# Kernel optimization log

Measured on AMD Instinct MI355X. Metric: run time of the kernel, lower is better.

Reference implementation:

```python
import jax, jax.numpy as jnp
import numpy as np

PS = 8          # patch_size
NF = 64         # num_feat
HEADS = 1
HW = 64         # hard-coded spatial size (Fold output_size=(64,64))
DIM = PS * PS * NF          # 4096
HID = DIM // HEADS          # 4096
NPATCH = (HW // PS) ** 2    # 64


def conv2d(x, w, b, groups=1):
    # x: [N,C,H,W], w: [O, C//groups, 3, 3], padding=1 stride=1 == SAME
    y = jax.lax.conv_general_dilated(
        x, w, window_strides=(1, 1), padding='SAME',
        dimension_numbers=('NCHW', 'OIHW', 'NCHW'),
        feature_group_count=groups)
    return y + b[None, :, None, None]


def unfold(x):
    # nn.Unfold(kernel=PS, stride=PS): [N,C,64,64] -> [N, C*PS*PS, NPATCH]
    N, C = x.shape[0], x.shape[1]
    g = HW // PS
    x = x.reshape(N, C, g, PS, g, PS)          # [N,C,gh,pi,gw,pj]
    x = x.transpose(0, 1, 3, 5, 2, 4)          # [N,C,pi,pj,gh,gw]
    return x.reshape(N, C * PS * PS, g * g)


def fold(y):
    # nn.Fold(output=(64,64), kernel=PS, stride=PS): inverse of unfold (non-overlapping)
    N = y.shape[0]
    g = HW // PS
    y = y.reshape(N, NF, PS, PS, g, g)         # [N,C,pi,pj,gh,gw]
    y = y.transpose(0, 1, 4, 2, 5, 3)          # [N,C,gh,pi,gw,pj]
    return y.reshape(N, NF, HW, HW)


def setup_inputs() -> dict:
    key = jax.random.key(0)
    ks = jax.random.split(key, 9)
    b, t = 4, 16
    x = jax.random.normal(ks[0], (b, t, NF, HW, HW), dtype=jnp.float32)
    s_dw = 1.0 / np.sqrt(9.0)          # depthwise: fan_in = 1*3*3
    s_fc = 1.0 / np.sqrt(NF * 9.0)     # full conv: fan_in = 64*3*3
    qw = jax.random.normal(ks[1], (NF, 1, 3, 3), jnp.float32) * s_dw
    qb = jax.random.normal(ks[2], (NF,), jnp.float32) * 0.01
    kw = jax.random.normal(ks[3], (NF, 1, 3, 3), jnp.float32) * s_dw
    kb = jax.random.normal(ks[4], (NF,), jnp.float32) * 0.01
    vw = jax.random.normal(ks[5], (NF, NF, 3, 3), jnp.float32) * s_fc
    vb = jax.random.normal(ks[6], (NF,), jnp.float32) * 0.01
    cw = jax.random.normal(ks[7], (NF, NF, 3, 3), jnp.float32) * s_fc
    cb = jax.random.normal(ks[8], (NF,), jnp.float32) * 0.01
    return {"x": x, "qw": qw, "qb": qb, "kw": kw, "kb": kb,
            "vw": vw, "vb": vb, "cw": cw, "cb": cb}


def reference(x, qw, qb, kw, kb, vw, vb, cw, cb):
    b, t, c, h, w = x.shape
    H, d, n = HEADS, HID, NPATCH
    xf = x.reshape(b * t, c, h, w)
    q = conv2d(xf, qw, qb, groups=NF)   # depthwise
    k = conv2d(xf, kw, kb, groups=NF)   # depthwise
    v = conv2d(xf, vw, vb)              # full conv
    # unfold -> [b,t,H,d,n] -> [b,H,d,t*n]
    def to_tokens(z):
        z = unfold(z).reshape(b, t, H, d, n)
        return z.transpose(0, 2, 3, 1, 4).reshape(b, H, d, t * n)
    uq, uk, uv = to_tokens(q), to_tokens(k), to_tokens(v)
    attn = jnp.einsum('bhdi,bhdj->bhij', uq, uk) * (d ** -0.5)
    attn = jax.nn.softmax(attn, axis=-1)
    ax = jnp.einsum('bhij,bhdj->bhid', attn, uv)          # [b,H,t*n,d]
    ax = ax.reshape(b, H, t, n, d).transpose(0, 2, 1, 4, 3)  # [b,t,H,d,n]
    ax = ax.reshape(b * t, DIM, n)
    feat = fold(ax)                                        # [b*t,C,64,64]
    out = conv2d(feat, cw, cb).reshape(x.shape)
    return out + x
```

## Files before the change

kernel.cpp:

```cpp
#include <hip/hip_runtime.h>

typedef unsigned short u16;
typedef unsigned int   u32;

typedef __bf16 bf16_t;
typedef bf16_t bf16x8 __attribute__((ext_vector_type(8)));
typedef float  f32x4  __attribute__((ext_vector_type(4)));

__device__ __forceinline__ float bf2f(u16 h) { return __uint_as_float(((u32)h) << 16); }
__device__ __forceinline__ u16 f2bf(float f) {
    u32 u = __float_as_uint(f);
    u32 r = u + 0x7fffu + ((u >> 16) & 1u);
    return (u16)(r >> 16);
}
__device__ __forceinline__ void unpack2(u32 v, float& a, float& b) {
    a = __uint_as_float(v << 16);
    b = __uint_as_float(v & 0xffff0000u);
}


__global__ __launch_bounds__(256) void dwconv_qk(
    const float* __restrict__ x, const float* __restrict__ qw, const float* __restrict__ qb,
    const float* __restrict__ kw, const float* __restrict__ kb,
    u16* __restrict__ qtok, u16* __restrict__ ktok)
{
    __shared__ float ts[64][65];
    int img = blockIdx.x >> 6, c = blockIdx.x & 63;
    int tid = threadIdx.x;
    const float* xp = x + ((size_t)((img << 6) + c) << 12);
    #pragma unroll
    for (int i = 0; i < 4; i++) {
        int p = i * 1024 + tid * 4;
        int r = p >> 6, col = p & 63;
        float4 v = *(const float4*)(xp + p);
        ts[r][col] = v.x; ts[r][col + 1] = v.y; ts[r][col + 2] = v.z; ts[r][col + 3] = v.w;
    }
    float qwv[9], kwv[9];
    #pragma unroll
    for (int i = 0; i < 9; i++) { qwv[i] = qw[c * 9 + i]; kwv[i] = kw[c * 9 + i]; }
    float qbb = qb[c], kbb = kb[c];
    __syncthreads();

    int r = tid >> 2, q = tid & 3;
    int b = img >> 4, t = img & 15;
    int gh = r >> 3, pr = r & 7;
    size_t base = (((size_t)(b << 10) + (t << 6) + (gh << 3)) << 12) + (c << 6) + (pr << 3);

    #pragma unroll
    for (int s = 0; s < 2; s++) {
        int gw = q * 2 + s, w0 = gw << 3;
        float qa[8], ka[8];
        #pragma unroll
        for (int i = 0; i < 8; i++) { qa[i] = qbb; ka[i] = kbb; }
        #pragma unroll
        for (int ky = 0; ky < 3; ky++) {
            int hh = r + ky - 1;
            if (hh < 0 || hh > 63) continue;
            float xr[10];
            #pragma unroll
            for (int cc = 0; cc < 10; cc++) {
                int ww = w0 - 1 + cc;
                xr[cc] = (ww < 0 || ww > 63) ? 0.f : ts[hh][ww];
            }
            #pragma unroll
            for (int kx = 0; kx < 3; kx++) {
                float wq = qwv[ky * 3 + kx], wk = kwv[ky * 3 + kx];
                #pragma unroll
                for (int i = 0; i < 8; i++) {
                    qa[i] += xr[i + kx] * wq;
                    ka[i] += xr[i + kx] * wk;
                }
            }
        }
        union { u16 h8[8]; uint4 u; } pq, pk;
        #pragma unroll
        for (int i = 0; i < 8; i++) { pq.h8[i] = f2bf(qa[i]); pk.h8[i] = f2bf(ka[i]); }
        size_t o = base + ((size_t)gw << 12);
        *(uint4*)&qtok[o] = pq.u;
        *(uint4*)&ktok[o] = pk.u;
    }
}

__global__ __launch_bounds__(256) void nchw_to_nhwc(
    const float* __restrict__ x, u16* __restrict__ xb)
{
    __shared__ float ts[64][65];
    int img = blockIdx.x >> 6, h = blockIdx.x & 63;
    int tid = threadIdx.x;
    const float* xp = x + ((size_t)img << 18) + (h << 6);
    int c = tid >> 2, wg = (tid & 3) << 4;
    #pragma unroll
    for (int i = 0; i < 4; i++) {
        float4 v = *(const float4*)(xp + ((size_t)c << 12) + wg + i * 4);
        ts[c][wg + i * 4 + 0] = v.x; ts[c][wg + i * 4 + 1] = v.y;
        ts[c][wg + i * 4 + 2] = v.z; ts[c][wg + i * 4 + 3] = v.w;
    }
    __syncthreads();
    int w = tid >> 2, cg = (tid & 3) << 4;
    union { u16 h8[8]; uint4 u; } p0, p1;
    #pragma unroll
    for (int m = 0; m < 8; m++) {
        p0.h8[m] = f2bf(ts[cg + m][w]);
        p1.h8[m] = f2bf(ts[cg + 8 + m][w]);
    }
    u16* dst = xb + (((((size_t)img << 6) + h) << 6) + w) * 64 + cg;
    *(uint4*)dst       = p0.u;
    *(uint4*)(dst + 8) = p1.u;
}

__global__ __launch_bounds__(256) void weight_prep2(
    const float* __restrict__ vw, const float* __restrict__ cw, u16* __restrict__ wt)
{
    int e = blockIdx.x * 256 + threadIdx.x;
    if (e >= 73728) return;
    int half = e >= 36864;
    int e2 = e - (half ? 36864 : 0);
    int tap = e2 >> 12;
    int kbg = (e2 >> 9) & 7;
    int cout = (e2 >> 3) & 63;
    int s = e2 & 7;
    int cin = (kbg << 3) + s;
    const float* src = half ? cw : vw;
    wt[e] = f2bf(src[((cout << 6) + cin) * 9 + tap]);
}

template<bool IS_C>
__global__ __launch_bounds__(256, 2) void conv_mfma(
    const u16* __restrict__ xb, const u16* __restrict__ wt,
    const float* __restrict__ bias, const float* __restrict__ xres,
    u16* __restrict__ vt, float* __restrict__ out)
{
    __shared__ u16 xs[21120];
    __shared__ u16 wl[18432];

    int tid = threadIdx.x, lane = tid & 63, wv = tid >> 6;
    int img = blockIdx.x >> 3, rowblk = blockIdx.x & 7;
    int h0 = rowblk << 3;
    int r16 = lane & 15, kb = lane >> 4;

    const uint4 z4 = make_uint4(0, 0, 0, 0);
    for (int i = tid; i < 80; i += 256) {
        int r = i >> 3, k = i & 7;
        *(uint4*)&xs[r * 2112 + 2048 + k * 8] = z4;
    }
    if (rowblk == 0)
        for (int i = tid; i < 264; i += 256) *(uint4*)&xs[i * 8] = z4;
    if (rowblk == 7)
        for (int i = tid; i < 264; i += 256) *(uint4*)&xs[9 * 2112 + i * 8] = z4;

    int pxoff[4][3];
    #pragma unroll
    for (int g = 0; g < 4; g++) {
        #pragma unroll
        for (int dx = 0; dx < 3; dx++) {
            int cc = g * 16 + r16 + dx - 1;
            int off;
            if (cc < 0)        off = 2048 + kb * 8;
            else if (cc >= 64) off = 2080 + kb * 8;
            else               off = (cc >> 4) * 512 + kb * 128 + (cc & 15) * 8;
            pxoff[g][dx] = off;
        }
    }

    const u16* xb_i = xb + ((size_t)img << 18);

    f32x4 acc[4][8] = {};

    for (int c0 = 0; c0 < 64; c0 += 32) {
        __syncthreads();
        #pragma unroll
        for (int k = 0; k < 10; k++) {
            int i = wv + (k << 2);
            int r = i >> 2, g = i & 3;
            int h = h0 + r - 1;
            if (h >= 0 && h < 64) {
                const u16* src = xb_i + (size_t)(((h << 6) + (g << 4) + r16) << 6)
                                 + c0 + (kb << 3);
                u16* dst = xs + r * 2112 + g * 512;
                __builtin_amdgcn_global_load_lds(
                    (const __attribute__((address_space(1))) u32*)src,
                    (__attribute__((address_space(3))) u32*)dst, 16, 0, 0);
            }
        }
        #pragma unroll
        for (int tp = 0; tp < 9; tp++) {
            const u16* srcw = wt + tp * 4096 + (c0 << 6) + tid * 8;
            u16* dstw = wl + tp * 2048 + (wv << 9);
            __builtin_amdgcn_global_load_lds(
                (const __attribute__((address_space(1))) u32*)srcw,
                (__attribute__((address_space(3))) u32*)dstw, 16, 0, 0);
        }
        __syncthreads();

        #pragma unroll
        for (int dy = 0; dy < 3; dy++) {
            #pragma unroll
            for (int dx = 0; dx < 3; dx++) {
                int tap = dy * 3 + dx;
                bf16x8 af[4];
                #pragma unroll
                for (int m = 0; m < 4; m++)
                    af[m] = *(const bf16x8*)&wl[tap * 2048 + (kb << 9)
                                                + (((m << 4) + r16) << 3)];
                #pragma unroll
                for (int nf = 0; nf < 8; nf++) {
                    int rowb = ((wv << 1) + (nf >> 2) + dy) * 2112;
                    bf16x8 bv = *(const bf16x8*)&xs[rowb + pxoff[nf & 3][dx]];
                    #pragma unroll
                    for (int m = 0; m < 4; m++)
                        acc[m][nf] = __builtin_amdgcn_mfma_f32_16x16x32_bf16(
                            af[m], bv, acc[m][nf], 0, 0, 0);
                }
            }
        }
    }

    int b = img >> 4, t = img & 15;
    if constexpr (!IS_C) {
        __syncthreads();
        u16* wbuf = xs + (wv << 12);
        int j0 = (t << 6) + (rowblk << 3);
        #pragma unroll
        for (int mh = 0; mh < 2; mh++) {
            #pragma unroll
            for (int mm = 0; mm < 2; mm++) {
                int m = mh * 2 + mm;
                #pragma unroll
                for (int q = 0; q < 4; q++) {
                    int cm = mm * 16 + (kb << 2) + q;
                    float bvs = bias[mh * 32 + cm];
                    #pragma unroll
                    for (int nf = 0; nf < 8; nf++) {
                        int lrL = nf >> 2;
                        int pc  = r16 & 7;
                        int gw  = ((nf & 3) << 1) | (r16 >> 3);
                        wbuf[(((cm << 1) | lrL) << 6) + (pc << 3) + gw] =
                            f2bf(acc[m][nf][q] + bvs);
                    }
                }
            }
            #pragma unroll
            for (int it = 0; it < 8; it++) {
                int cid = it * 64 + lane;
                int cm  = cid >> 4;
                int lrL = (cid >> 3) & 1;
                int pc  = cid & 7;
                int lr  = (wv << 1) | lrL;
                int cout = mh * 32 + cm;
                int dd  = (((lr << 3) | pc) << 6) | cout;
                uint4 val = *(uint4*)&wbuf[cid << 3];
                *(uint4*)&vt[(((size_t)((b << 12) + dd)) << 10) + j0] = val;
            }
            if (mh == 0) __syncthreads();
        }
    } else {
        #pragma unroll
        for (int m = 0; m < 4; m++) {
            #pragma unroll
            for (int q = 0; q < 4; q++) {
                int cout = (m << 4) + (kb << 2) + q;
                float bvs = bias[cout];
                #pragma unroll
                for (int nf = 0; nf < 8; nf++) {
                    int lr = (wv << 1) + (nf >> 2);
                    int w = (nf & 3) * 16 + r16;
                    int h = h0 + lr;
                    size_t o = ((size_t)((img << 6) + cout) << 12) + (h << 6) + w;
                    out[o] = acc[m][nf][q] + bvs + xres[o];
                }
            }
        }
    }
}

template<int TM, int TN, int LDA, int LDB, int LDC, int KTOT, int MT, int NT,
         int EPI, int OCC>
__global__ __launch_bounds__(256, OCC) void mfma_abt(
    const u16* __restrict__ Ag, const u16* __restrict__ Bg,
    const float* __restrict__ invl, u16* __restrict__ Cg)
{
    constexpr int MF = TM / 32;
    constexpr int NF = TN / 32;
    constexpr int KSTEPS = KTOT / 64;
    constexpr int NWG = 4 * MT * NT;
    constexpr int CPX = NWG / 8;
    __shared__ u16 As[2][TM * 64];
    __shared__ u16 Bs[2][TN * 64];

    int tid  = threadIdx.x;
    int lane = tid & 63, wv = tid >> 6;
    int bid  = blockIdx.x;
    int id   = (bid & 7) * CPX + (bid >> 3);
    int nt   = id % NT;
    int rest = id / NT;
    int mt   = rest % MT;
    int bi   = rest / MT;

    const u16* Ab = Ag + (size_t)bi * (1024 * (size_t)LDA) + (size_t)(mt * TM) * LDA;
    const u16* Bb = Bg + (size_t)bi * ((size_t)NT * TN * LDB) + (size_t)(nt * TN) * LDB;

    int srow = tid >> 3;
    int slot = tid & 7;
    int wr = wv >> 1, wc = wv & 1;
    int r16 = lane & 15, kb = lane >> 4;

    f32x4 acc[MF][NF] = {};

    auto STAGE = [&](int bsel, int k0) {
        #pragma unroll
        for (int it = 0; it < MF; it++) {
            int rl = it * 32 + srow;
            int kg = slot ^ (rl & 7);
            const u16* sa = Ab + (size_t)rl * LDA + k0 + kg * 8;
            u16* da = &As[bsel][it * 2048 + wv * 512];
            __builtin_amdgcn_global_load_lds(
                (const __attribute__((address_space(1))) u32*)sa,
                (__attribute__((address_space(3))) u32*)da, 16, 0, 0);
        }
        #pragma unroll
        for (int it = 0; it < NF; it++) {
            int rl = it * 32 + srow;
            int kg = slot ^ (rl & 7);
            const u16* sb = Bb + (size_t)rl * LDB + k0 + kg * 8;
            u16* db = &Bs[bsel][it * 2048 + wv * 512];
            __builtin_amdgcn_global_load_lds(
                (const __attribute__((address_space(1))) u32*)sb,
                (__attribute__((address_space(3))) u32*)db, 16, 0, 0);
        }
    };

    STAGE(0, 0);
    __syncthreads();

    for (int s = 0; s < KSTEPS; s++) {
        int cur = s & 1;
        if (s + 1 < KSTEPS) STAGE(cur ^ 1, (s + 1) * 64);
        #pragma unroll
        for (int kk = 0; kk < 2; kk++) {
            bf16x8 af[MF], bfr[NF];
            #pragma unroll
            for (int m = 0; m < MF; m++) {
                int row  = wr * (TM / 2) + m * 16 + r16;
                int boff = row * 128 + (((kk * 32 + kb * 8) * 2) ^ ((row & 7) << 4));
                af[m] = *(const bf16x8*)((const char*)&As[cur][0] + boff);
            }
            #pragma unroll
            for (int n = 0; n < NF; n++) {
                int row  = wc * (TN / 2) + n * 16 + r16;
                int boff = row * 128 + (((kk * 32 + kb * 8) * 2) ^ ((row & 7) << 4));
                bfr[n] = *(const bf16x8*)((const char*)&Bs[cur][0] + boff);
            }
            #pragma unroll
            for (int m = 0; m < MF; m++)
                #pragma unroll
                for (int n = 0; n < NF; n++)
                    acc[m][n] = __builtin_amdgcn_mfma_f32_16x16x32_bf16(
                        af[m], bfr[n], acc[m][n], 0, 0, 0);
        }
        __syncthreads();
    }

    size_t crow0 = (size_t)bi * 1024 + (size_t)mt * TM + wr * (TM / 2);
    int col0 = nt * TN + wc * (TN / 2);
    #pragma unroll
    for (int m = 0; m < MF; m++) {
        float il[4] = {1.f, 1.f, 1.f, 1.f};
        if constexpr (EPI == 2) {
            #pragma unroll
            for (int q = 0; q < 4; q++)
                il[q] = invl[crow0 + m * 16 + kb * 4 + q];
        }
        #pragma unroll
        for (int n = 0; n < NF; n++) {
            #pragma unroll
            for (int q = 0; q < 4; q++) {
                int i_loc = m * 16 + kb * 4 + q;
                int j     = col0 + n * 16 + r16;
                float v   = acc[m][n][q];
                if constexpr (EPI == 0) {
                    Cg[(crow0 + i_loc) * (size_t)LDC + j] = f2bf(__expf(v * 0.015625f));
                } else {
                    int i2 = mt * TM + wr * (TM / 2) + i_loc;
                    int t = i2 >> 6, patch = i2 & 63;
                    int c = j & 63, pr = (j >> 9) & 7, pc = (j >> 6) & 7;
                    int hh = ((patch >> 3) << 3) + pr, w2 = ((patch & 7) << 3) + pc;
                    size_t o = ((((size_t)(bi * 16 + t) << 6) + hh) << 6) + w2;
                    Cg[(o << 6) + c] = f2bf(v * il[q]);
                }
            }
        }
    }
}

__global__ __launch_bounds__(256) void rowsum_inv_kernel(
    const u16* __restrict__ p, float* __restrict__ invl)
{
    int row = blockIdx.x, tid = threadIdx.x;
    uint2 v = ((const uint2*)(p + ((size_t)row << 10)))[tid];
    float a, b, c, d;
    unpack2(v.x, a, b); unpack2(v.y, c, d);
    float s = (a + b) + (c + d);
    #pragma unroll
    for (int off = 32; off; off >>= 1) s += __shfl_xor(s, off);
    __shared__ float rs[4];
    if ((tid & 63) == 0) rs[tid >> 6] = s;
    __syncthreads();
    if (tid == 0) invl[row] = 1.f / ((rs[0] + rs[1]) + (rs[2] + rs[3]));
}

extern "C" void kernel_launch(void* const* d_in, const int* in_sizes, int n_in,
                              void* d_out, int out_size, void* d_ws, size_t ws_size,
                              hipStream_t stream)
{
    const float* x  = (const float*)d_in[0];
    const float* qw = (const float*)d_in[1];
    const float* qb = (const float*)d_in[2];
    const float* kw = (const float*)d_in[3];
    const float* kb = (const float*)d_in[4];
    const float* vw = (const float*)d_in[5];
    const float* vb = (const float*)d_in[6];
    const float* cw = (const float*)d_in[7];
    const float* cb = (const float*)d_in[8];
    float* out = (float*)d_out;

    char* ws = (char*)d_ws;
    u16*   qtok  = (u16*)d_out;
    u16*   ktok  = (u16*)ws;
    u16*   probs = (u16*)(ws + (size_t)32 * 1024 * 1024);
    float* invl  = (float*)(ws + (size_t)40 * 1024 * 1024);
    u16*   wtv   = (u16*)(ws + (size_t)40 * 1024 * 1024 + 65536);
    u16*   wtc   = wtv + 36864;
    u16*   xbuf  = ktok;
    u16*   vt    = qtok;
    u16*   axb   = ktok;

    weight_prep2<<<288, 256, 0, stream>>>(vw, cw, wtv);

    dwconv_qk<<<4096, 256, 0, stream>>>(x, qw, qb, kw, kb, qtok, ktok);

    mfma_abt<64, 128, 4096, 4096, 1024, 4096, 16, 8, 0, 3><<<512, 256, 0, stream>>>(
        qtok, ktok, nullptr, probs);

    rowsum_inv_kernel<<<4096, 256, 0, stream>>>(probs, invl);

    nchw_to_nhwc<<<4096, 256, 0, stream>>>(x, xbuf);

    conv_mfma<false><<<512, 256, 0, stream>>>(xbuf, wtv, vb, nullptr, vt, nullptr);

    mfma_abt<128, 128, 1024, 1024, 4096, 1024, 8, 32, 2, 2><<<1024, 256, 0, stream>>>(
        probs, vt, invl, axb);

    conv_mfma<true><<<512, 256, 0, stream>>>(axb, wtc, cb, x, nullptr, out);
}
```

Before: 323.0 us.

## Fuse softmax row sums into QK GEMM, single-buffer LDS, remap conv blocks

The exp-score GEMM epilogue now accumulates per-row sums of the rounded probabilities and adds them into a zeroed buffer with atomics. This removes the separate rowsum kernel and its re-read of the probability matrix. The GEMMs drop LDS double buffering in favour of one buffer synchronised twice per step, and their occupancy hints change (3→2 and 2→4). The conv kernels also remap block indices to spread images across XCDs. Single buffering lowers LDS use to allow higher occupancy, but it loses the overlap of global loads with MFMA work.

```diff
diff --git a/kernel.cpp b/kernel.cpp
--- a/kernel.cpp
+++ b/kernel.cpp
@@ -134,7 +134,9 @@
     __shared__ u16 wl[18432];
 
     int tid = threadIdx.x, lane = tid & 63, wv = tid >> 6;
-    int img = blockIdx.x >> 3, rowblk = blockIdx.x & 7;
+    int bid = blockIdx.x;
+    int virt = (bid & 7) * 64 + (bid >> 3);
+    int img = virt >> 3, rowblk = virt & 7;
     int h0 = rowblk << 3;
     int r16 = lane & 15, kb = lane >> 4;
 
@@ -277,15 +279,14 @@
          int EPI, int OCC>
 __global__ __launch_bounds__(256, OCC) void mfma_abt(
     const u16* __restrict__ Ag, const u16* __restrict__ Bg,
-    const float* __restrict__ invl, u16* __restrict__ Cg)
+    float* __restrict__ rs, u16* __restrict__ Cg)
 {
     constexpr int MF = TM / 32;
     constexpr int NF = TN / 32;
-    constexpr int KSTEPS = KTOT / 64;
     constexpr int NWG = 4 * MT * NT;
     constexpr int CPX = NWG / 8;
-    __shared__ u16 As[2][TM * 64];
-    __shared__ u16 Bs[2][TN * 64];
+    __shared__ u16 As[TM * 64];
+    __shared__ u16 Bs[TN * 64];
 
     int tid  = threadIdx.x;
     int lane = tid & 63, wv = tid >> 6;
@@ -306,13 +307,14 @@
 
     f32x4 acc[MF][NF] = {};
 
-    auto STAGE = [&](int bsel, int k0) {
+    for (int k0 = 0; k0 < KTOT; k0 += 64) {
+        __syncthreads();
         #pragma unroll
         for (int it = 0; it < MF; it++) {
             int rl = it * 32 + srow;
             int kg = slot ^ (rl & 7);
             const u16* sa = Ab + (size_t)rl * LDA + k0 + kg * 8;
-            u16* da = &As[bsel][it * 2048 + wv * 512];
+            u16* da = As + it * 2048 + wv * 512;
             __builtin_amdgcn_global_load_lds(
                 (const __attribute__((address_space(1))) u32*)sa,
                 (__attribute__((address_space(3))) u32*)da, 16, 0, 0);
@@ -322,19 +324,13 @@
             int rl = it * 32 + srow;
             int kg = slot ^ (rl & 7);
             const u16* sb = Bb + (size_t)rl * LDB + k0 + kg * 8;
-            u16* db = &Bs[bsel][it * 2048 + wv * 512];
+            u16* db = Bs + it * 2048 + wv * 512;
             __builtin_amdgcn_global_load_lds(
                 (const __attribute__((address_space(1))) u32*)sb,
                 (__attribute__((address_space(3))) u32*)db, 16, 0, 0);
         }
-    };
-
-    STAGE(0, 0);
-    __syncthreads();
-
-    for (int s = 0; s < KSTEPS; s++) {
-        int cur = s & 1;
-        if (s + 1 < KSTEPS) STAGE(cur ^ 1, (s + 1) * 64);
+        __syncthreads();
+
         #pragma unroll
         for (int kk = 0; kk < 2; kk++) {
             bf16x8 af[MF], bfr[NF];
@@ -342,13 +338,13 @@
             for (int m = 0; m < MF; m++) {
                 int row  = wr * (TM / 2) + m * 16 + r16;
                 int boff = row * 128 + (((kk * 32 + kb * 8) * 2) ^ ((row & 7) << 4));
-                af[m] = *(const bf16x8*)((const char*)&As[cur][0] + boff);
+                af[m] = *(const bf16x8*)((const char*)As + boff);
             }
             #pragma unroll
             for (int n = 0; n < NF; n++) {
                 int row  = wc * (TN / 2) + n * 16 + r16;
                 int boff = row * 128 + (((kk * 32 + kb * 8) * 2) ^ ((row & 7) << 4));
-                bfr[n] = *(const bf16x8*)((const char*)&Bs[cur][0] + boff);
+                bfr[n] = *(const bf16x8*)((const char*)Bs + boff);
             }
             #pragma unroll
             for (int m = 0; m < MF; m++)
@@ -357,29 +353,44 @@
                     acc[m][n] = __builtin_amdgcn_mfma_f32_16x16x32_bf16(
                         af[m], bfr[n], acc[m][n], 0, 0, 0);
         }
-        __syncthreads();
     }
 
     size_t crow0 = (size_t)bi * 1024 + (size_t)mt * TM + wr * (TM / 2);
     int col0 = nt * TN + wc * (TN / 2);
-    #pragma unroll
-    for (int m = 0; m < MF; m++) {
-        float il[4] = {1.f, 1.f, 1.f, 1.f};
-        if constexpr (EPI == 2) {
+    if constexpr (EPI == 0) {
+        #pragma unroll
+        for (int m = 0; m < MF; m++) {
+            #pragma unroll
+            for (int q = 0; q < 4; q++) {
+                size_t row = crow0 + m * 16 + kb * 4 + q;
+                float rsum = 0.f;
+                #pragma unroll
+                for (int n = 0; n < NF; n++) {
+                    float e = __expf(acc[m][n][q] * 0.015625f);
+                    u16 pv = f2bf(e);
+                    rsum += bf2f(pv);
+                    Cg[row * (size_t)LDC + col0 + n * 16 + r16] = pv;
+                }
+                #pragma unroll
+                for (int off = 1; off < 16; off <<= 1)
+                    rsum += __shfl_xor(rsum, off);
+                if (r16 == 0) atomicAdd(&rs[row], rsum);
+            }
+        }
+    } else {
+        #pragma unroll
+        for (int m = 0; m < MF; m++) {
+            float il[4];
             #pragma unroll
             for (int q = 0; q < 4; q++)
-                il[q] = invl[crow0 + m * 16 + kb * 4 + q];
-        }
-        #pragma unroll
-        for (int n = 0; n < NF; n++) {
-            #pragma unroll
-            for (int q = 0; q < 4; q++) {
-                int i_loc = m * 16 + kb * 4 + q;
-                int j     = col0 + n * 16 + r16;
-                float v   = acc[m][n][q];
-                if constexpr (EPI == 0) {
-                    Cg[(crow0 + i_loc) * (size_t)LDC + j] = f2bf(__expf(v * 0.015625f));
-                } else {
+                il[q] = 1.0f / rs[crow0 + m * 16 + kb * 4 + q];
+            #pragma unroll
+            for (int n = 0; n < NF; n++) {
+                #pragma unroll
+                for (int q = 0; q < 4; q++) {
+                    int i_loc = m * 16 + kb * 4 + q;
+                    int j     = col0 + n * 16 + r16;
+                    float v   = acc[m][n][q];
                     int i2 = mt * TM + wr * (TM / 2) + i_loc;
                     int t = i2 >> 6, patch = i2 & 63;
                     int c = j & 63, pr = (j >> 9) & 7, pc = (j >> 6) & 7;
@@ -390,22 +401,6 @@
             }
         }
     }
-}
-
-__global__ __launch_bounds__(256) void rowsum_inv_kernel(
-    const u16* __restrict__ p, float* __restrict__ invl)
-{
-    int row = blockIdx.x, tid = threadIdx.x;
-    uint2 v = ((const uint2*)(p + ((size_t)row << 10)))[tid];
-    float a, b, c, d;
-    unpack2(v.x, a, b); unpack2(v.y, c, d);
-    float s = (a + b) + (c + d);
-    #pragma unroll
-    for (int off = 32; off; off >>= 1) s += __shfl_xor(s, off);
-    __shared__ float rs[4];
-    if ((tid & 63) == 0) rs[tid >> 6] = s;
-    __syncthreads();
-    if (tid == 0) invl[row] = 1.f / ((rs[0] + rs[1]) + (rs[2] + rs[3]));
 }
 
 extern "C" void kernel_launch(void* const* d_in, const int* in_sizes, int n_in,
@@ -427,7 +422,7 @@
     u16*   qtok  = (u16*)d_out;
     u16*   ktok  = (u16*)ws;
     u16*   probs = (u16*)(ws + (size_t)32 * 1024 * 1024);
-    float* invl  = (float*)(ws + (size_t)40 * 1024 * 1024);
+    float* rowsum= (float*)(ws + (size_t)40 * 1024 * 1024);
     u16*   wtv   = (u16*)(ws + (size_t)40 * 1024 * 1024 + 65536);
     u16*   wtc   = wtv + 36864;
     u16*   xbuf  = ktok;
@@ -438,17 +433,17 @@
 
     dwconv_qk<<<4096, 256, 0, stream>>>(x, qw, qb, kw, kb, qtok, ktok);
 
-    mfma_abt<64, 128, 4096, 4096, 1024, 4096, 16, 8, 0, 3><<<512, 256, 0, stream>>>(
-        qtok, ktok, nullptr, probs);
-
-    rowsum_inv_kernel<<<4096, 256, 0, stream>>>(probs, invl);
+    hipMemsetAsync(rowsum, 0, 4096 * sizeof(float), stream);
+
+    mfma_abt<64, 128, 4096, 4096, 1024, 4096, 16, 8, 0, 2><<<512, 256, 0, stream>>>(
+        qtok, ktok, rowsum, probs);
 
     nchw_to_nhwc<<<4096, 256, 0, stream>>>(x, xbuf);
 
     conv_mfma<false><<<512, 256, 0, stream>>>(xbuf, wtv, vb, nullptr, vt, nullptr);
 
-    mfma_abt<128, 128, 1024, 1024, 4096, 1024, 8, 32, 2, 2><<<1024, 256, 0, stream>>>(
-        probs, vt, invl, axb);
+    mfma_abt<128, 128, 1024, 1024, 4096, 1024, 8, 32, 2, 4><<<1024, 256, 0, stream>>>(
+        probs, vt, rowsum, axb);
 
     conv_mfma<true><<<512, 256, 0, stream>>>(axb, wtc, cb, x, nullptr, out);
 }
```

Result: faster. 302.4 us (-6.4%).
